# Performance work log

Hardware: AMD Instinct MI355X
Metric: run time of the kernel (lower is better)

Reference implementation:

```python
import jax, jax.numpy as jnp
import numpy as np

N_NODES = 50000
N_EDGES = 600000
D_IN = 128
D_HID = 128


def _graph_conv(x, src, dst, W, b, n_nodes):
    # DGL GraphConv with norm='both': out = D_in^{-1/2} A (D_out^{-1/2} x) W + b
    ones = jnp.ones(src.shape[0], dtype=x.dtype)
    deg_out = jnp.maximum(jax.ops.segment_sum(ones, src, num_segments=n_nodes), 1.0)
    deg_in = jnp.maximum(jax.ops.segment_sum(ones, dst, num_segments=n_nodes), 1.0)
    h = x * (deg_out ** -0.5)[:, None]            # [N, d] scale by src-side norm
    agg = jax.ops.segment_sum(h[src], dst, num_segments=n_nodes)  # SpMM aggregate
    agg = agg * (deg_in ** -0.5)[:, None]
    return agg @ W + b


def _two_layer(x, src, dst, W1, b1, W2, b2):
    h = jax.nn.relu(_graph_conv(x, src, dst, W1, b1, N_NODES))
    return jax.nn.relu(_graph_conv(h, src, dst, W2, b2, N_NODES))


def setup_inputs() -> dict:
    key = jax.random.key(0)
    ks = jax.random.split(key, 16)
    inp = {}
    for i in range(4):
        inp[f"x{i+1}"] = jax.random.normal(ks[3 * i], (N_NODES, D_IN), dtype=jnp.float32)
        inp[f"src{i+1}"] = jax.random.randint(ks[3 * i + 1], (N_EDGES,), 0, N_NODES)
        inp[f"dst{i+1}"] = jax.random.randint(ks[3 * i + 2], (N_EDGES,), 0, N_NODES)
    inp["W1"] = jax.random.normal(ks[12], (D_IN, D_HID), dtype=jnp.float32) * (D_IN ** -0.5)
    inp["b1"] = jnp.zeros((D_HID,), dtype=jnp.float32)
    inp["W2"] = jax.random.normal(ks[13], (D_HID, D_HID), dtype=jnp.float32) * (D_HID ** -0.5)
    inp["b2"] = jnp.zeros((D_HID,), dtype=jnp.float32)
    return inp


def reference(x1, src1, dst1, x2, src2, dst2, x3, src3, dst3, x4, src4, dst4,
              W1, b1, W2, b2):
    h1 = _two_layer(x1, src1, dst1, W1, b1, W2, b2)
    h2 = _two_layer(x2, src2, dst2, W1, b1, W2, b2)
    h3 = _two_layer(x3, src3, dst3, W1, b1, W2, b2)
    h4 = _two_layer(x4, src4, dst4, W1, b1, W2, b2)
    # multi_graph_opt='mean': concat along node axis, mean over nodes -> [D_HID]
    x = jnp.mean(jnp.concatenate([h1, h2, h3, h4], axis=0), axis=0)
    # output_opt='mean': scalar
    return jnp.mean(x)
```

## Files before the change

kernel.cpp:

```cpp
#include <hip/hip_runtime.h>
#include <hip/hip_bf16.h>

#define N_NODES 50000
#define N_EDGES 600000
#define D 128

#define NBUCK 64
#define BUCK_R 782
#define BCAP 16384
#define EPB 2048

typedef __attribute__((ext_vector_type(8))) short bf16x8;
typedef __attribute__((ext_vector_type(4))) float f32x4;

__device__ __forceinline__ const int* pick4(const int* a, const int* b,
                                            const int* c, const int* d, int g) {
    return g == 0 ? a : g == 1 ? b : g == 2 ? c : d;
}
__device__ __forceinline__ const float4* pick4f(const float4* a, const float4* b,
                                                const float4* c, const float4* d, int g) {
    return g == 0 ? a : g == 1 ? b : g == 2 ? c : d;
}

__device__ __forceinline__ unsigned bfpair(float a, float b) {
    unsigned ua = __float_as_uint(a); ua = (ua + 0x7FFF + ((ua >> 16) & 1)) >> 16;
    unsigned ub = __float_as_uint(b); ub = (ub + 0x7FFF + ((ub >> 16) & 1)) >> 16;
    return ua | (ub << 16);
}
__device__ __forceinline__ unsigned short f2bf(float x) {
    unsigned u = __float_as_uint(x); u = (u + 0x7FFF + ((u >> 16) & 1)) >> 16;
    return (unsigned short)u;
}

__global__ __launch_bounds__(256) void phaseA_kernel(
        const int* s0, const int* s1, const int* s2, const int* s3,
        const int* d0, const int* d1, const int* d2, const int* d3,
        int* __restrict__ bCurD, int* __restrict__ bCurS,
        int* __restrict__ pairs, unsigned short* __restrict__ svals, int nEdges) {
    int gi = blockIdx.y;
    const int* src = pick4(s0, s1, s2, s3, gi);
    const int* dst = pick4(d0, d1, d2, d3, gi);
    int* pg = pairs + (size_t)gi * NBUCK * BCAP;
    unsigned short* sg = svals + (size_t)gi * NBUCK * BCAP;

    __shared__ int cntD[64], cntS[64], gposD[64], gposS[64], lcurD[64], lcurS[64];
    int t = threadIdx.x;
    if (t < 64) { cntD[t] = 0; cntS[t] = 0; }
    __syncthreads();

    int myD[8], myS[8];
    int base = blockIdx.x * EPB + t;
    #pragma unroll
    for (int j = 0; j < 8; ++j) {
        int e = base + j * 256;
        if (e < nEdges) {
            myD[j] = dst[e]; myS[j] = src[e];
            atomicAdd(&cntD[myD[j] / BUCK_R], 1);
            atomicAdd(&cntS[myS[j] / BUCK_R], 1);
        } else myD[j] = -1;
    }
    __syncthreads();
    if (t < 64) {
        int c = cntD[t];
        gposD[t] = t * BCAP + (c ? atomicAdd(&bCurD[gi * 64 + t], c) : 0);
        lcurD[t] = 0;
        c = cntS[t];
        gposS[t] = t * BCAP + (c ? atomicAdd(&bCurS[gi * 64 + t], c) : 0);
        lcurS[t] = 0;
    }
    __syncthreads();
    #pragma unroll
    for (int j = 0; j < 8; ++j) {
        if (myD[j] >= 0) {
            int bD = myD[j] / BUCK_R, bS = myS[j] / BUCK_R;
            int lp = atomicAdd(&lcurD[bD], 1);
            pg[gposD[bD] + lp] = ((myD[j] - bD * BUCK_R) << 16) | myS[j];
            int ls = atomicAdd(&lcurS[bS], 1);
            sg[gposS[bS] + ls] = (unsigned short)(myS[j] - bS * BUCK_R);
        }
    }
}

__global__ __launch_bounds__(256) void csrB_kernel(
        const int* __restrict__ bCurD, const int* __restrict__ pairs,
        int* __restrict__ rowptrBase, int* __restrict__ eixBase,
        float* __restrict__ rsIBase) {
    int gi = blockIdx.y, b = blockIdx.x;
    int* rowptr = rowptrBase + (size_t)gi * (N_NODES + 1);
    int* eidx = eixBase + (size_t)gi * N_EDGES;
    float* rsI = rsIBase + (size_t)gi * N_NODES;
    const int* pg = pairs + ((size_t)gi * NBUCK + b) * BCAP;
    const int* bCur = bCurD + gi * 64;

    __shared__ int P[BCAP];
    __shared__ int cnt[1024];
    __shared__ int cur[1024];
    __shared__ int wpart[4];
    __shared__ int sbase;

    int t = threadIdx.x;
    int nb = bCur[b]; if (nb > BCAP) nb = BCAP;

    if (t < 64) {
        int v = (t < b) ? min(bCur[t], BCAP) : 0;
        for (int off = 32; off; off >>= 1) v += __shfl_down(v, off, 64);
        if (t == 0) sbase = v;
    }
    for (int i = t; i < 1024; i += 256) cnt[i] = 0;
    __syncthreads();
    int base = sbase;

    for (int i = t; i < nb; i += 256) {
        int p = pg[i];
        P[i] = p;
        atomicAdd(&cnt[p >> 16], 1);
    }
    __syncthreads();

    int c0 = cnt[t * 4 + 0], c1 = cnt[t * 4 + 1], c2 = cnt[t * 4 + 2], c3 = cnt[t * 4 + 3];
    int ts = c0 + c1 + c2 + c3;
    int lane = t & 63, w = t >> 6;
    int incl = ts;
    for (int off = 1; off < 64; off <<= 1) {
        int u = __shfl_up(incl, off, 64);
        if (lane >= off) incl += u;
    }
    if (lane == 63) wpart[w] = incl;
    __syncthreads();
    int wb = 0;
    #pragma unroll
    for (int i = 0; i < 4; ++i) if (i < w) wb += wpart[i];
    int ex = wb + incl - ts;
    cur[t * 4 + 0] = ex;
    cur[t * 4 + 1] = ex + c0;
    cur[t * 4 + 2] = ex + c0 + c1;
    cur[t * 4 + 3] = ex + c0 + c1 + c2;
    __syncthreads();

    int lo = b * BUCK_R;
    int nh = N_NODES - lo; if (nh > BUCK_R) nh = BUCK_R;
    for (int i = t; i < nh; i += 256) {
        rowptr[lo + i] = base + cur[i];
        rsI[lo + i] = 1.0f / sqrtf(fmaxf((float)cnt[i], 1.0f));
    }
    if (b == NBUCK - 1 && t == 0) rowptr[N_NODES] = N_EDGES;
    __syncthreads();

    for (int i = t; i < nb; i += 256) {
        int p = P[i];
        int pos = atomicAdd(&cur[p >> 16], 1);
        eidx[base + pos] = p & 0xFFFF;
    }
}

__global__ __launch_bounds__(256) void csrC_kernel(
        const int* __restrict__ bCurS, const unsigned short* __restrict__ svals,
        float* __restrict__ rsOBase) {
    int gi = blockIdx.y, b = blockIdx.x;
    float* rsO = rsOBase + (size_t)gi * N_NODES;
    const unsigned short* sg = svals + ((size_t)gi * NBUCK + b) * BCAP;
    __shared__ int cnt[1024];
    int t = threadIdx.x;
    for (int i = t; i < 1024; i += 256) cnt[i] = 0;
    __syncthreads();
    int ns = bCurS[gi * 64 + b]; if (ns > BCAP) ns = BCAP;
    for (int i = t; i < ns; i += 256) atomicAdd(&cnt[sg[i]], 1);
    __syncthreads();
    int lo = b * BUCK_R;
    int nh = N_NODES - lo; if (nh > BUCK_R) nh = BUCK_R;
    for (int i = t; i < nh; i += 256)
        rsO[lo + i] = 1.0f / sqrtf(fmaxf((float)cnt[i], 1.0f));
}

__global__ void wconv_kernel(const float* __restrict__ W1, const float* __restrict__ W2,
                             unsigned* __restrict__ Wp1, unsigned* __restrict__ Wp2) {
    const float* W = blockIdx.y ? W2 : W1;
    unsigned* Wp = blockIdx.y ? Wp2 : Wp1;
    int o = blockIdx.x * 256 + threadIdx.x;
    int j2 = o & 3, lane = (o >> 2) & 63, nt = (o >> 8) & 7, kc = o >> 11;
    int k = kc * 32 + (lane >> 4) * 8 + j2 * 2;
    int col = nt * 16 + (lane & 15);
    Wp[o] = bfpair(W[k * 128 + col], W[(k + 1) * 128 + col]);
}

__global__ void xconv_kernel(const float4* x0, const float4* x1,
                             const float4* x2, const float4* x3,
                             const float* __restrict__ rsOBase,
                             uint4* __restrict__ xbBase, int gFirst, int n ) {
    int gi = blockIdx.y;
    const float4* x = pick4f(x0, x1, x2, x3, gFirst + gi);
    const float* rsO = rsOBase + (size_t)(gFirst + gi) * N_NODES;
    uint4* xb = xbBase + (size_t)gi * (N_NODES * 16);
    int i = blockIdx.x * blockDim.x + threadIdx.x;
    if (i >= n) return;
    float sc = rsO[i >> 4];
    float4 a = x[i * 2];
    float4 b = x[i * 2 + 1];
    uint4 o;
    o.x = bfpair(a.x * sc, a.y * sc);
    o.y = bfpair(a.z * sc, a.w * sc);
    o.z = bfpair(b.x * sc, b.y * sc);
    o.w = bfpair(b.z * sc, b.w * sc);
    xb[i] = o;
}

#define NCHUNK 3125
template <int LAYER>
__global__ __launch_bounds__(256) void fused_kernel(
        const int* __restrict__ rowptrBase, const int* __restrict__ eixBase,
        const unsigned short* __restrict__ hBase,
        const float* __restrict__ rsIBase, const float* __restrict__ rsOBase,
        const uint4* __restrict__ Wp, const float* __restrict__ bias,
        unsigned short* __restrict__ outBase, double* __restrict__ acc, int gFirst) {
    const int gi = blockIdx.y;
    const int g = gFirst + gi;
    const int* rowptr = rowptrBase + (size_t)g * (N_NODES + 1);
    const int* eidx   = eixBase + (size_t)g * N_EDGES;
    const float* rsI  = rsIBase + (size_t)g * N_NODES;
    const float* rsO  = rsOBase + (size_t)g * N_NODES;
    const unsigned short* h = hBase + (size_t)gi * N_NODES * D;
    unsigned short* outb = outBase + (size_t)gi * N_NODES * D;

    __shared__ unsigned short A[16][136];

    const int t = threadIdx.x;
    const int row = t >> 4;
    const int sub = t & 15;
    const int lane = t & 63, wv = t >> 6;
    const int l15 = lane & 15, lh = lane >> 4;

    bf16x8 bfr[4][2];
    #pragma unroll
    for (int kc = 0; kc < 4; ++kc)
        #pragma unroll
        for (int j = 0; j < 2; ++j) {
            uint4 u = Wp[(kc * 8 + wv * 2 + j) * 64 + lane];
            bfr[kc][j] = *(bf16x8*)&u;
        }
    float bv[2];
    #pragma unroll
    for (int j = 0; j < 2; ++j) bv[j] = bias[wv * 32 + j * 16 + l15];

    double lsum = 0.0;

    for (int ch = blockIdx.x; ch < NCHUNK; ch += gridDim.x) {
        const int r = ch * 16 + row;
        float a[8] = {0.f, 0.f, 0.f, 0.f, 0.f, 0.f, 0.f, 0.f};
        int p = rowptr[r], pend = rowptr[r + 1];
        const unsigned short* hp = h + sub * 8;
        for (; p + 2 <= pend; p += 2) {
            uint4 u = *(const uint4*)(hp + (size_t)eidx[p] * 128);
            uint4 v = *(const uint4*)(hp + (size_t)eidx[p + 1] * 128);
            a[0] += __uint_as_float(u.x << 16);  a[1] += __uint_as_float(u.x & 0xFFFF0000u);
            a[2] += __uint_as_float(u.y << 16);  a[3] += __uint_as_float(u.y & 0xFFFF0000u);
            a[4] += __uint_as_float(u.z << 16);  a[5] += __uint_as_float(u.z & 0xFFFF0000u);
            a[6] += __uint_as_float(u.w << 16);  a[7] += __uint_as_float(u.w & 0xFFFF0000u);
            a[0] += __uint_as_float(v.x << 16);  a[1] += __uint_as_float(v.x & 0xFFFF0000u);
            a[2] += __uint_as_float(v.y << 16);  a[3] += __uint_as_float(v.y & 0xFFFF0000u);
            a[4] += __uint_as_float(v.z << 16);  a[5] += __uint_as_float(v.z & 0xFFFF0000u);
            a[6] += __uint_as_float(v.w << 16);  a[7] += __uint_as_float(v.w & 0xFFFF0000u);
        }
        if (p < pend) {
            uint4 u = *(const uint4*)(hp + (size_t)eidx[p] * 128);
            a[0] += __uint_as_float(u.x << 16);  a[1] += __uint_as_float(u.x & 0xFFFF0000u);
            a[2] += __uint_as_float(u.y << 16);  a[3] += __uint_as_float(u.y & 0xFFFF0000u);
            a[4] += __uint_as_float(u.z << 16);  a[5] += __uint_as_float(u.z & 0xFFFF0000u);
            a[6] += __uint_as_float(u.w << 16);  a[7] += __uint_as_float(u.w & 0xFFFF0000u);
        }
        {
            float sc = rsI[r];
            uint4 pk;
            pk.x = bfpair(a[0] * sc, a[1] * sc);
            pk.y = bfpair(a[2] * sc, a[3] * sc);
            pk.z = bfpair(a[4] * sc, a[5] * sc);
            pk.w = bfpair(a[6] * sc, a[7] * sc);
            *(uint4*)&A[row][sub * 8] = pk;
        }
        __syncthreads();

        bf16x8 afr[4];
        #pragma unroll
        for (int kc = 0; kc < 4; ++kc) {
            uint4 u = *(const uint4*)&A[l15][kc * 32 + lh * 8];
            afr[kc] = *(bf16x8*)&u;
        }
        __syncthreads();

        f32x4 c[2];
        c[0] = (f32x4){0.f, 0.f, 0.f, 0.f};
        c[1] = (f32x4){0.f, 0.f, 0.f, 0.f};
        #pragma unroll
        for (int kc = 0; kc < 4; ++kc) {
            c[0] = __builtin_amdgcn_mfma_f32_16x16x32_bf16(afr[kc], bfr[kc][0], c[0], 0, 0, 0);
            c[1] = __builtin_amdgcn_mfma_f32_16x16x32_bf16(afr[kc], bfr[kc][1], c[1], 0, 0, 0);
        }

        const int r0 = ch * 16 + lh * 4;
        if (LAYER == 2) {
            #pragma unroll
            for (int jj = 0; jj < 4; ++jj) {
                lsum += (double)fmaxf(c[0][jj] + bv[0], 0.f)
                      + (double)fmaxf(c[1][jj] + bv[1], 0.f);
            }
        } else {
            #pragma unroll
            for (int jj = 0; jj < 4; ++jj) {
                float sc = rsO[r0 + jj];
                outb[(size_t)(r0 + jj) * 128 + wv * 32 + l15]      = f2bf(fmaxf(c[0][jj] + bv[0], 0.f) * sc);
                outb[(size_t)(r0 + jj) * 128 + wv * 32 + 16 + l15] = f2bf(fmaxf(c[1][jj] + bv[1], 0.f) * sc);
            }
        }
    }

    if (LAYER == 2) {
        for (int off = 32; off; off >>= 1) lsum += __shfl_down(lsum, off, 64);
        __shared__ double wred[4];
        if (lane == 0) wred[wv] = lsum;
        __syncthreads();
        if (t == 0) atomicAdd(acc, wred[0] + wred[1] + wred[2] + wred[3]);
    }
}

__global__ void finalize_kernel(const double* __restrict__ acc, float* __restrict__ out) {
    if (threadIdx.x == 0 && blockIdx.x == 0)
        out[0] = (float)(acc[0] / (4.0 * N_NODES * D));
}

extern "C" void kernel_launch(void* const* d_in, const int* in_sizes, int n_in,
                              void* d_out, int out_size, void* d_ws, size_t ws_size,
                              hipStream_t stream) {
    const float* x[4];
    const int* src[4];
    const int* dst[4];
    for (int g = 0; g < 4; ++g) {
        x[g]   = (const float*)d_in[3 * g + 0];
        src[g] = (const int*)  d_in[3 * g + 1];
        dst[g] = (const int*)  d_in[3 * g + 2];
    }
    const float* W1 = (const float*)d_in[12];
    const float* b1 = (const float*)d_in[13];
    const float* W2 = (const float*)d_in[14];
    const float* b2 = (const float*)d_in[15];
    float* out = (float*)d_out;

    int* ws32 = (int*)d_ws;
    double* acc     = (double*)d_ws;
    int* bCurD      = ws32 + 64;
    int* bCurS      = ws32 + 320;
    unsigned* Wp1   = (unsigned*)(ws32 + 1024);
    unsigned* Wp2   = Wp1 + 8192;
    int* rowptrBase = ws32 + 17408;
    float* rsIBase  = (float*)(ws32 + 217412);
    float* rsOBase  = (float*)(ws32 + 417412);
    int* eixBase    = ws32 + 617412;
    int* pairs      = ws32 + 3017412;
    unsigned short* svals = (unsigned short*)(pairs + 4194304);
    unsigned short* xbA   = (unsigned short*)(ws32 + 3017412);

    auto needBytes = [](int gb) -> size_t {
        size_t ov = (size_t)gb * 6400000;
        if (ov < 6291456) ov = 6291456;
        return (3017412 + ov) * 4;
    };
    int gb = 1;
    if (ws_size >= needBytes(4)) gb = 4;
    else if (ws_size >= needBytes(2)) gb = 2;
    unsigned short* AbA = xbA + (size_t)gb * N_NODES * D;

    const int paGrid    = (N_EDGES + EPB - 1) / EPB;
    const int xconvGrid = (N_NODES * 16 + 255) / 256;
    const int fusedGrid = 1563;

    hipMemsetAsync(d_ws, 0, 1024 * sizeof(int), stream);

    wconv_kernel<<<dim3(32, 2), 256, 0, stream>>>(W1, W2, Wp1, Wp2);
    phaseA_kernel<<<dim3(paGrid, 4), 256, 0, stream>>>(
        src[0], src[1], src[2], src[3], dst[0], dst[1], dst[2], dst[3],
        bCurD, bCurS, pairs, svals, N_EDGES);
    csrB_kernel<<<dim3(NBUCK, 4), 256, 0, stream>>>(
        bCurD, pairs, rowptrBase, eixBase, rsIBase);
    csrC_kernel<<<dim3(NBUCK, 4), 256, 0, stream>>>(bCurS, svals, rsOBase);

    for (int g0 = 0; g0 < 4; g0 += gb) {
        int nb = 4 - g0 < gb ? 4 - g0 : gb;
        xconv_kernel<<<dim3(xconvGrid, nb), 256, 0, stream>>>(
            (const float4*)x[0], (const float4*)x[1], (const float4*)x[2], (const float4*)x[3],
            rsOBase, (uint4*)xbA, g0, N_NODES * 16);
        fused_kernel<1><<<dim3(fusedGrid, nb), 256, 0, stream>>>(
            rowptrBase, eixBase, xbA, rsIBase, rsOBase,
            (const uint4*)Wp1, b1, AbA, nullptr, g0);
        fused_kernel<2><<<dim3(fusedGrid, nb), 256, 0, stream>>>(
            rowptrBase, eixBase, AbA, rsIBase, rsOBase,
            (const uint4*)Wp2, b2, nullptr, acc, g0);
    }

    finalize_kernel<<<1, 64, 0, stream>>>(acc, out);
}
```

Before: 348.0 us.

## Split features into 32-column slabs and process 64-row chunks per block

Node features are now stored as four column-quarter slabs of 32 bf16 values per node. Each fused block handles 64 rows and runs four gather passes, one per slab, feeding MFMA as it goes. Launches are now one grid per graph, with one block per chunk instead of a grid-stride loop. The goal is a smaller per-pass gather working set that fits cache better and more rows of MFMA work per block. The cost is that the edge index list is read four times per row, and per-graph launches are serialized where graphs previously ran in a single batched launch.

```diff
diff --git a/kernel.cpp b/kernel.cpp
--- a/kernel.cpp
+++ b/kernel.cpp
@@ -9,6 +9,9 @@
 #define BUCK_R 782
 #define BCAP 16384
 #define EPB 2048
+
+#define CH_ROWS 64
+#define NCH ((N_NODES + CH_ROWS - 1) / CH_ROWS)
 
 typedef __attribute__((ext_vector_type(8))) short bf16x8;
 typedef __attribute__((ext_vector_type(4))) float f32x4;
@@ -193,7 +196,10 @@
     uint4* xb = xbBase + (size_t)gi * (N_NODES * 16);
     int i = blockIdx.x * blockDim.x + threadIdx.x;
     if (i >= n) return;
-    float sc = rsO[i >> 4];
+    int r = i >> 4;
+    int q = (i >> 2) & 3;
+    int s = i & 3;
+    float sc = rsO[r];
     float4 a = x[i * 2];
     float4 b = x[i * 2 + 1];
     uint4 o;
@@ -201,31 +207,22 @@
     o.y = bfpair(a.z * sc, a.w * sc);
     o.z = bfpair(b.x * sc, b.y * sc);
     o.w = bfpair(b.z * sc, b.w * sc);
-    xb[i] = o;
-}
-
-#define NCHUNK 3125
+    xb[((size_t)q * N_NODES + r) * 4 + s] = o;
+}
+
 template <int LAYER>
 __global__ __launch_bounds__(256) void fused_kernel(
-        const int* __restrict__ rowptrBase, const int* __restrict__ eixBase,
-        const unsigned short* __restrict__ hBase,
-        const float* __restrict__ rsIBase, const float* __restrict__ rsOBase,
+        const int* __restrict__ rowptr, const int* __restrict__ eidx,
+        const unsigned short* __restrict__ h,
+        const float* __restrict__ rsI, const float* __restrict__ rsO,
         const uint4* __restrict__ Wp, const float* __restrict__ bias,
-        unsigned short* __restrict__ outBase, double* __restrict__ acc, int gFirst) {
-    const int gi = blockIdx.y;
-    const int g = gFirst + gi;
-    const int* rowptr = rowptrBase + (size_t)g * (N_NODES + 1);
-    const int* eidx   = eixBase + (size_t)g * N_EDGES;
-    const float* rsI  = rsIBase + (size_t)g * N_NODES;
-    const float* rsO  = rsOBase + (size_t)g * N_NODES;
-    const unsigned short* h = hBase + (size_t)gi * N_NODES * D;
-    unsigned short* outb = outBase + (size_t)gi * N_NODES * D;
-
-    __shared__ unsigned short A[16][136];
+        unsigned short* __restrict__ outb,
+        double* __restrict__ acc) {
+    __shared__ unsigned short A[CH_ROWS][40];
 
     const int t = threadIdx.x;
-    const int row = t >> 4;
-    const int sub = t & 15;
+    const int row = t >> 2;
+    const int sub = t & 3;
     const int lane = t & 63, wv = t >> 6;
     const int l15 = lane & 15, lh = lane >> 4;
 
@@ -241,16 +238,27 @@
     #pragma unroll
     for (int j = 0; j < 2; ++j) bv[j] = bias[wv * 32 + j * 16 + l15];
 
-    double lsum = 0.0;
-
-    for (int ch = blockIdx.x; ch < NCHUNK; ch += gridDim.x) {
-        const int r = ch * 16 + row;
+    const int ch = blockIdx.x;
+    const int r = ch * CH_ROWS + row;
+    int p0 = 0, p1 = 0;
+    float sc = 0.f;
+    if (r < N_NODES) { p0 = rowptr[r]; p1 = rowptr[r + 1]; sc = rsI[r]; }
+
+    f32x4 c[4][2];
+    #pragma unroll
+    for (int rt = 0; rt < 4; ++rt) {
+        c[rt][0] = (f32x4){0.f, 0.f, 0.f, 0.f};
+        c[rt][1] = (f32x4){0.f, 0.f, 0.f, 0.f};
+    }
+
+    #pragma unroll
+    for (int q = 0; q < 4; ++q) {
         float a[8] = {0.f, 0.f, 0.f, 0.f, 0.f, 0.f, 0.f, 0.f};
-        int p = rowptr[r], pend = rowptr[r + 1];
-        const unsigned short* hp = h + sub * 8;
-        for (; p + 2 <= pend; p += 2) {
-            uint4 u = *(const uint4*)(hp + (size_t)eidx[p] * 128);
-            uint4 v = *(const uint4*)(hp + (size_t)eidx[p + 1] * 128);
+        const unsigned short* hq = h + (size_t)q * (N_NODES * 32) + sub * 8;
+        int p = p0;
+        for (; p + 2 <= p1; p += 2) {
+            uint4 u = *(const uint4*)(hq + (size_t)eidx[p] * 32);
+            uint4 v = *(const uint4*)(hq + (size_t)eidx[p + 1] * 32);
             a[0] += __uint_as_float(u.x << 16);  a[1] += __uint_as_float(u.x & 0xFFFF0000u);
             a[2] += __uint_as_float(u.y << 16);  a[3] += __uint_as_float(u.y & 0xFFFF0000u);
             a[4] += __uint_as_float(u.z << 16);  a[5] += __uint_as_float(u.z & 0xFFFF0000u);
@@ -260,15 +268,14 @@
             a[4] += __uint_as_float(v.z << 16);  a[5] += __uint_as_float(v.z & 0xFFFF0000u);
             a[6] += __uint_as_float(v.w << 16);  a[7] += __uint_as_float(v.w & 0xFFFF0000u);
         }
-        if (p < pend) {
-            uint4 u = *(const uint4*)(hp + (size_t)eidx[p] * 128);
+        if (p < p1) {
+            uint4 u = *(const uint4*)(hq + (size_t)eidx[p] * 32);
             a[0] += __uint_as_float(u.x << 16);  a[1] += __uint_as_float(u.x & 0xFFFF0000u);
             a[2] += __uint_as_float(u.y << 16);  a[3] += __uint_as_float(u.y & 0xFFFF0000u);
             a[4] += __uint_as_float(u.z << 16);  a[5] += __uint_as_float(u.z & 0xFFFF0000u);
             a[6] += __uint_as_float(u.w << 16);  a[7] += __uint_as_float(u.w & 0xFFFF0000u);
         }
         {
-            float sc = rsI[r];
             uint4 pk;
             pk.x = bfpair(a[0] * sc, a[1] * sc);
             pk.y = bfpair(a[2] * sc, a[3] * sc);
@@ -278,36 +285,33 @@
         }
         __syncthreads();
 
-        bf16x8 afr[4];
         #pragma unroll
-        for (int kc = 0; kc < 4; ++kc) {
-            uint4 u = *(const uint4*)&A[l15][kc * 32 + lh * 8];
-            afr[kc] = *(bf16x8*)&u;
+        for (int rt = 0; rt < 4; ++rt) {
+            uint4 u = *(const uint4*)&A[rt * 16 + l15][lh * 8];
+            bf16x8 afr = *(bf16x8*)&u;
+            c[rt][0] = __builtin_amdgcn_mfma_f32_16x16x32_bf16(afr, bfr[q][0], c[rt][0], 0, 0, 0);
+            c[rt][1] = __builtin_amdgcn_mfma_f32_16x16x32_bf16(afr, bfr[q][1], c[rt][1], 0, 0, 0);
         }
         __syncthreads();
-
-        f32x4 c[2];
-        c[0] = (f32x4){0.f, 0.f, 0.f, 0.f};
-        c[1] = (f32x4){0.f, 0.f, 0.f, 0.f};
+    }
+
+    double lsum = 0.0;
+    #pragma unroll
+    for (int rt = 0; rt < 4; ++rt) {
         #pragma unroll
-        for (int kc = 0; kc < 4; ++kc) {
-            c[0] = __builtin_amdgcn_mfma_f32_16x16x32_bf16(afr[kc], bfr[kc][0], c[0], 0, 0, 0);
-            c[1] = __builtin_amdgcn_mfma_f32_16x16x32_bf16(afr[kc], bfr[kc][1], c[1], 0, 0, 0);
-        }
-
-        const int r0 = ch * 16 + lh * 4;
-        if (LAYER == 2) {
-            #pragma unroll
-            for (int jj = 0; jj < 4; ++jj) {
-                lsum += (double)fmaxf(c[0][jj] + bv[0], 0.f)
-                      + (double)fmaxf(c[1][jj] + bv[1], 0.f);
-            }
-        } else {
-            #pragma unroll
-            for (int jj = 0; jj < 4; ++jj) {
-                float sc = rsO[r0 + jj];
-                outb[(size_t)(r0 + jj) * 128 + wv * 32 + l15]      = f2bf(fmaxf(c[0][jj] + bv[0], 0.f) * sc);
-                outb[(size_t)(r0 + jj) * 128 + wv * 32 + 16 + l15] = f2bf(fmaxf(c[1][jj] + bv[1], 0.f) * sc);
+        for (int jj = 0; jj < 4; ++jj) {
+            int rowE = ch * CH_ROWS + rt * 16 + lh * 4 + jj;
+            if (rowE < N_NODES) {
+                float o0 = fmaxf(c[rt][0][jj] + bv[0], 0.f);
+                float o1 = fmaxf(c[rt][1][jj] + bv[1], 0.f);
+                if (LAYER == 2) {
+                    lsum += (double)o0 + (double)o1;
+                } else {
+                    float s2 = rsO[rowE];
+                    size_t bse = ((size_t)wv * N_NODES + rowE) * 32;
+                    outb[bse + l15]      = f2bf(o0 * s2);
+                    outb[bse + 16 + l15] = f2bf(o1 * s2);
+                }
             }
         }
     }
@@ -369,7 +373,6 @@
 
     const int paGrid    = (N_EDGES + EPB - 1) / EPB;
     const int xconvGrid = (N_NODES * 16 + 255) / 256;
-    const int fusedGrid = 1563;
 
     hipMemsetAsync(d_ws, 0, 1024 * sizeof(int), stream);
 
@@ -386,12 +389,19 @@
         xconv_kernel<<<dim3(xconvGrid, nb), 256, 0, stream>>>(
             (const float4*)x[0], (const float4*)x[1], (const float4*)x[2], (const float4*)x[3],
             rsOBase, (uint4*)xbA, g0, N_NODES * 16);
-        fused_kernel<1><<<dim3(fusedGrid, nb), 256, 0, stream>>>(
-            rowptrBase, eixBase, xbA, rsIBase, rsOBase,
-            (const uint4*)Wp1, b1, AbA, nullptr, g0);
-        fused_kernel<2><<<dim3(fusedGrid, nb), 256, 0, stream>>>(
-            rowptrBase, eixBase, AbA, rsIBase, rsOBase,
-            (const uint4*)Wp2, b2, nullptr, acc, g0);
+        for (int g = g0; g < g0 + nb; ++g) {
+            int li = g - g0;
+            const int* rowptr = rowptrBase + (size_t)g * (N_NODES + 1);
+            const int* eidx   = eixBase + (size_t)g * N_EDGES;
+            const float* rsI  = rsIBase + (size_t)g * N_NODES;
+            const float* rsO  = rsOBase + (size_t)g * N_NODES;
+            const unsigned short* xb = xbA + (size_t)li * N_NODES * D;
+            unsigned short* Ab       = AbA + (size_t)li * N_NODES * D;
+            fused_kernel<1><<<NCH, 256, 0, stream>>>(
+                rowptr, eidx, xb, rsI, rsO, (const uint4*)Wp1, b1, Ab, nullptr);
+            fused_kernel<2><<<NCH, 256, 0, stream>>>(
+                rowptr, eidx, Ab, rsI, nullptr, (const uint4*)Wp2, b2, nullptr, acc);
+        }
     }
 
     finalize_kernel<<<1, 64, 0, stream>>>(acc, out);
```

Result: slower. 630.9 us (+81.3%).
